# Optimization experiments

Measured on AMD Instinct MI355X. Metric: run time of the kernel, lower is better.

Reference implementation:

```python
import jax, jax.numpy as jnp
import numpy as np

D_MODEL = 2048
NUM_HEADS = 16
HEAD_DIM = D_MODEL // NUM_HEADS
SEQ = 2048
BATCH = 2
ROPE_BASE = 10000.0
EPS = 1e-5


def _rope_cache(seq_len, head_dim, base):
    inv_freq = 1.0 / (base ** (jnp.arange(0, head_dim, 2, dtype=jnp.float32) / head_dim))
    t = jnp.arange(seq_len, dtype=jnp.float32)
    freqs = jnp.outer(t, inv_freq)                      # [S, hd/2]
    emb = jnp.concatenate([freqs, freqs], axis=-1)      # [S, hd]
    return jnp.cos(emb), jnp.sin(emb)


def _rotate_half(x):
    x1, x2 = jnp.split(x, 2, axis=-1)
    return jnp.concatenate([-x2, x1], axis=-1)


def setup_inputs() -> dict:
    key = jax.random.key(0)
    ks = jax.random.split(key, 8)
    s = 1.0 / np.sqrt(D_MODEL)
    inp = {
        "x": jax.random.normal(ks[0], (SEQ, BATCH, D_MODEL), dtype=jnp.float32),
        "causal_mask": jnp.triu(jnp.ones((SEQ, SEQ), dtype=jnp.bool_), k=1),
        "key_padding_mask": jnp.zeros((BATCH, SEQ), dtype=jnp.bool_),
        "norm_w": jnp.ones((D_MODEL,), dtype=jnp.float32),
        "q_w": jax.random.normal(ks[1], (D_MODEL, D_MODEL), dtype=jnp.float32) * s,
        "q_b": jnp.zeros((D_MODEL,), dtype=jnp.float32),
        "k_w": jax.random.normal(ks[2], (D_MODEL, D_MODEL), dtype=jnp.float32) * s,
        "k_b": jnp.zeros((D_MODEL,), dtype=jnp.float32),
        "v_w": jax.random.normal(ks[3], (D_MODEL, D_MODEL), dtype=jnp.float32) * s,
        "v_b": jnp.zeros((D_MODEL,), dtype=jnp.float32),
        "o_w": jax.random.normal(ks[4], (D_MODEL, D_MODEL), dtype=jnp.float32) * s,
        "o_b": jnp.zeros((D_MODEL,), dtype=jnp.float32),
    }
    return inp


def reference(x, causal_mask, key_padding_mask, norm_w, q_w, q_b, k_w, k_b, v_w, v_b, o_w, o_b):
    seq_len, batch, _ = x.shape
    # RMSNorm variant: x / (||x||_2 + eps) * w  (note: L2 norm, not RMS)
    nrm = jnp.linalg.norm(x, axis=-1, keepdims=True)
    xn = x / (nrm + EPS) * norm_w

    q = (xn @ q_w.T + q_b).reshape(seq_len, batch, NUM_HEADS, HEAD_DIM)
    k = (xn @ k_w.T + k_b).reshape(seq_len, batch, NUM_HEADS, HEAD_DIM)
    v = (xn @ v_w.T + v_b).reshape(seq_len, batch, NUM_HEADS, HEAD_DIM)

    cos, sin = _rope_cache(seq_len, HEAD_DIM, ROPE_BASE)
    cos = cos[:, None, None, :]
    sin = sin[:, None, None, :]
    q = q * cos + _rotate_half(q) * sin
    k = k * cos + _rotate_half(k) * sin

    # [S,B,H,D] -> [B,H,S,D]
    q = q.transpose(1, 2, 0, 3)
    k = k.transpose(1, 2, 0, 3)
    v = v.transpose(1, 2, 0, 3)

    scores = jnp.einsum('bhqd,bhkd->bhqk', q, k) / jnp.sqrt(jnp.float32(HEAD_DIM))
    neg_inf = jnp.float32(-jnp.inf)
    scores = jnp.where(causal_mask[None, None, :, :], neg_inf, scores)
    scores = jnp.where(key_padding_mask[:, None, None, :], neg_inf, scores)

    attn = jax.nn.softmax(scores, axis=-1)
    out = jnp.einsum('bhqk,bhkd->bhqd', attn, v)
    out = out.transpose(2, 0, 1, 3).reshape(seq_len, batch, D_MODEL)  # [S,B,D]
    return out @ o_w.T + o_b
```

## Files before the change

### kernel.cpp

```cpp
#include <hip/hip_runtime.h>
#include <hip/hip_bf16.h>
#include <cstdint>

typedef __attribute__((ext_vector_type(8))) short short8_t;
typedef __attribute__((ext_vector_type(4))) short s16x4;
typedef __attribute__((ext_vector_type(4))) float f32x4;

#define SEQ 2048
#define BATCH 2
#define DM 2048
#define NH 16
#define HD 128
#define SCALE 0.08838834764831845f

__device__ __forceinline__ short f2bf(float f) {
    union { __hip_bfloat16 h; short s; } u; u.h = __float2bfloat16(f); return u.s;
}
__device__ __forceinline__ float bf2f(short s) {
    union { short s; __hip_bfloat16 h; } u; u.s = s; return __bfloat162float(u.h);
}

__global__ void rope_table_kernel(float* __restrict__ cosT, float* __restrict__ sinT) {
    int t = blockIdx.x;
    int i = threadIdx.x;
    float inv = exp2f(-(2.0f * (float)i / 128.0f) * log2f(10000.0f));
    float a = (float)t * inv;
    cosT[t * 64 + i] = cosf(a);
    sinT[t * 64 + i] = sinf(a);
}

__global__ void cast4_kernel(const float* __restrict__ qw, const float* __restrict__ kw,
                             const float* __restrict__ vw, const float* __restrict__ ow,
                             short* __restrict__ out) {
    const int per = DM * DM / 4;
    int i = blockIdx.x * blockDim.x + threadIdx.x;
    int stride = gridDim.x * blockDim.x;
    for (; i < 4 * per; i += stride) {
        int region = i / per;
        int off = i - region * per;
        const float* src = region == 0 ? qw : (region == 1 ? kw : (region == 2 ? vw : ow));
        float4 v = ((const float4*)src)[off];
        s16x4 o;
        o[0] = f2bf(v.x); o[1] = f2bf(v.y); o[2] = f2bf(v.z); o[3] = f2bf(v.w);
        ((s16x4*)(out + (size_t)region * DM * DM))[off] = o;
    }
}

__global__ void __launch_bounds__(256) norm_cast_kernel(const float* __restrict__ x,
                                                        const float* __restrict__ w,
                                                        short* __restrict__ xn) {
    __shared__ float red[4];
    int row = blockIdx.x;
    const float* xr = x + (size_t)row * DM;
    short* outr = xn + (size_t)row * DM;
    int t = threadIdx.x;
    float vals[8];
    float ss = 0.f;
#pragma unroll
    for (int i = 0; i < 8; ++i) { float v = xr[t + 256 * i]; vals[i] = v; ss += v * v; }
#pragma unroll
    for (int off = 1; off < 64; off <<= 1) ss += __shfl_xor(ss, off);
    int lane = t & 63, wv = t >> 6;
    if (lane == 0) red[wv] = ss;
    __syncthreads();
    float tot = red[0] + red[1] + red[2] + red[3];
    float inv = 1.f / (sqrtf(tot) + 1e-5f);
#pragma unroll
    for (int i = 0; i < 8; ++i)
        outr[t + 256 * i] = f2bf(vals[i] * inv * w[t + 256 * i]);
}


__device__ __forceinline__ void stage64(const short* __restrict__ G, int gRow0, int K, int kb,
                                        short* dstLds, int w, int lane) {
#pragma unroll
    for (int p = 0; p < 4; ++p) {
        int c = p * 256 + w * 64 + lane;
        int row = c >> 3;
        int slot = (c & 7) ^ (row & 7);
        const short* g = G + (size_t)(gRow0 + row) * K + kb + slot * 8;
        __builtin_amdgcn_global_load_lds((const __attribute__((address_space(1))) void*)g,
                                         (__attribute__((address_space(3))) void*)(dstLds + (p * 256 + w * 64) * 8),
                                         16, 0, 0);
    }
}

template <int MODE>
__global__ void __launch_bounds__(256) gemm_bt2(const short* __restrict__ A,
                                                const short* __restrict__ B,
                                                int N, int K,
                                                short* __restrict__ oq, short* __restrict__ ok,
                                                short* __restrict__ ov,
                                                const float* __restrict__ bq,
                                                const float* __restrict__ bk,
                                                const float* __restrict__ bv,
                                                float* __restrict__ outF,
                                                const float* __restrict__ bias) {
    __shared__ short As[128 * 64];
    __shared__ short Bs[128 * 64];
    const int tid = threadIdx.x;
    const int lane = tid & 63;
    const int w = tid >> 6;
    const int wr = w >> 1, wc = w & 1;
    const int brow = blockIdx.y * 128;
    const int bcol = blockIdx.x * 128;

    f32x4 acc[4][4];
#pragma unroll
    for (int i = 0; i < 4; ++i)
#pragma unroll
        for (int j = 0; j < 4; ++j) acc[i][j] = (f32x4){0.f, 0.f, 0.f, 0.f};

    const int fr = lane & 15;
    const int fs = lane >> 4;

    for (int kb = 0; kb < K; kb += 64) {
        stage64(A, brow, K, kb, As, w, lane);
        stage64(B, bcol, K, kb, Bs, w, lane);
        __syncthreads();

        short8_t af[4][2], bfv[4][2];
#pragma unroll
        for (int i = 0; i < 4; ++i) {
            int ar = wr * 64 + i * 16 + fr;
#pragma unroll
            for (int ks = 0; ks < 2; ++ks)
                af[i][ks] = *(const short8_t*)&As[ar * 64 + ((ks * 4 + fs) ^ (fr & 7)) * 8];
        }
#pragma unroll
        for (int j = 0; j < 4; ++j) {
            int br = wc * 64 + j * 16 + fr;
#pragma unroll
            for (int ks = 0; ks < 2; ++ks)
                bfv[j][ks] = *(const short8_t*)&Bs[br * 64 + ((ks * 4 + fs) ^ (fr & 7)) * 8];
        }
#pragma unroll
        for (int ks = 0; ks < 2; ++ks)
#pragma unroll
            for (int i = 0; i < 4; ++i)
#pragma unroll
                for (int j = 0; j < 4; ++j)
                    acc[i][j] = __builtin_amdgcn_mfma_f32_16x16x32_bf16(af[i][ks], bfv[j][ks], acc[i][j], 0, 0, 0);
        __syncthreads();
    }

    const int fq = (lane >> 4) * 4;
#pragma unroll
    for (int i = 0; i < 4; ++i) {
        int mrow = brow + wr * 64 + i * 16 + fq;
#pragma unroll
        for (int j = 0; j < 4; ++j) {
            int ncol = bcol + wc * 64 + j * 16 + fr;
            if (MODE == 0) {
                int which = ncol >> 11;
                int hl = ncol & 2047;
                int h = hl >> 7, d = hl & 127;
                const float* bp = which == 0 ? bq : (which == 1 ? bk : bv);
                short* dst = which == 0 ? oq : (which == 1 ? ok : ov);
                float bval = bp[hl];
#pragma unroll
                for (int jj = 0; jj < 4; ++jj) {
                    int m = mrow + jj;
                    int s = m >> 1, b = m & 1;
                    float v = acc[i][j][jj] + bval;
                    size_t idx;
                    if (which == 2)
                        idx = (((size_t)(b * NH + h)) * HD + d) * SEQ + s;
                    else
                        idx = (((size_t)(b * NH + h)) * SEQ + s) * HD + d;
                    dst[idx] = f2bf(v);
                }
            } else {
                float bval = bias[ncol];
#pragma unroll
                for (int jj = 0; jj < 4; ++jj) {
                    int m = mrow + jj;
                    outF[(size_t)m * N + ncol] = acc[i][j][jj] + bval;
                }
            }
        }
    }
}

__global__ void __launch_bounds__(256) rope_kernel(short* __restrict__ q, short* __restrict__ k,
                                                   const float* __restrict__ cosT,
                                                   const float* __restrict__ sinT) {
    int w = threadIdx.x >> 6, lane = threadIdx.x & 63;
    int idx = blockIdx.x * 4 + w;
    int s = idx & (SEQ - 1);
    size_t base = (size_t)idx * HD;
    float c = cosT[s * 64 + lane], sn = sinT[s * 64 + lane];
    float q1 = bf2f(q[base + lane]), q2 = bf2f(q[base + lane + 64]);
    q[base + lane] = f2bf(q1 * c - q2 * sn);
    q[base + lane + 64] = f2bf(q2 * c + q1 * sn);
    float k1 = bf2f(k[base + lane]), k2 = bf2f(k[base + lane + 64]);
    k[base + lane] = f2bf(k1 * c - k2 * sn);
    k[base + lane + 64] = f2bf(k2 * c + k1 * sn);
}

__global__ void __launch_bounds__(512) attn_kernel(const short* __restrict__ Q,
                                                   const short* __restrict__ K,
                                                   const short* __restrict__ V,
                                                   short* __restrict__ AO) {
    __shared__ short Kl[64 * 136];
    __shared__ short Vt[128 * 88];
    __shared__ short Pl[8][16 * 88];

    const int bh = blockIdx.x;
    const int qt = blockIdx.y;
    const int b = bh >> 4;
    const int h = bh & 15;
    const size_t base = (size_t)bh * (SEQ * HD);
    const int tid = threadIdx.x;
    const int lane = tid & 63;
    const int w = tid >> 6;
    const int fr = lane & 15;
    const int fk = (lane >> 4) * 8;
    const int fq = (lane >> 4) * 4;
    const int qbase = qt * 128 + w * 16;
    const int qg = qbase + fr;

    short8_t qf[4];
#pragma unroll
    for (int kc = 0; kc < 4; ++kc)
        qf[kc] = *(const short8_t*)&Q[base + (size_t)(qbase + fr) * HD + kc * 32 + fk];

    f32x4 acc[8];
#pragma unroll
    for (int dt = 0; dt < 8; ++dt) acc[dt] = (f32x4){0.f, 0.f, 0.f, 0.f};
    float m_r = -1e30f, l_r = 0.f;

    const int ktmax = qt * 2 + 1;
    for (int kt = 0; kt <= ktmax; ++kt) {
#pragma unroll
        for (int p = 0; p < 2; ++p) {
            int idx = p * 512 + tid;
            int r = idx >> 4;
            int c8 = (idx & 15) * 8;
            *(short8_t*)&Kl[r * 136 + c8] =
                *(const short8_t*)&K[base + (size_t)(kt * 64 + r) * HD + c8];
        }
#pragma unroll
        for (int p = 0; p < 2; ++p) {
            int idx = p * 512 + tid;
            int d = idx >> 3;
            int c8 = (idx & 7) * 8;
            *(short8_t*)&Vt[d * 88 + c8] =
                *(const short8_t*)&V[base + (size_t)d * SEQ + kt * 64 + c8];
        }
        __syncthreads();

        if (kt * 64 <= qbase + 15) {
            f32x4 st[4];
#pragma unroll
            for (int nt = 0; nt < 4; ++nt) {
                f32x4 a = (f32x4){0.f, 0.f, 0.f, 0.f};
#pragma unroll
                for (int kc = 0; kc < 4; ++kc) {
                    short8_t kf = *(const short8_t*)&Kl[(nt * 16 + fr) * 136 + kc * 32 + fk];
                    a = __builtin_amdgcn_mfma_f32_16x16x32_bf16(kf, qf[kc], a, 0, 0, 0);
                }
                st[nt] = a;
            }

            float rmax = -1e30f;
#pragma unroll
            for (int nt = 0; nt < 4; ++nt) {
#pragma unroll
                for (int jj = 0; jj < 4; ++jj) {
                    int kg = kt * 64 + nt * 16 + fq + jj;
                    float sv = st[nt][jj];
                    sv = (kg > qg) ? -1e30f : sv;
                    st[nt][jj] = sv;
                    rmax = fmaxf(rmax, sv);
                }
            }
            rmax = fmaxf(rmax, __shfl_xor(rmax, 16));
            rmax = fmaxf(rmax, __shfl_xor(rmax, 32));
            float m_new = fmaxf(m_r, rmax);
            float corr = __expf((m_r - m_new) * SCALE);
            float rsum = 0.f;
#pragma unroll
            for (int nt = 0; nt < 4; ++nt) {
                s16x4 pk;
#pragma unroll
                for (int jj = 0; jj < 4; ++jj) {
                    float p = __expf((st[nt][jj] - m_new) * SCALE);
                    rsum += p;
                    pk[jj] = f2bf(p);
                }
                *(s16x4*)&Pl[w][fr * 88 + nt * 16 + fq] = pk;
            }
            rsum += __shfl_xor(rsum, 16);
            rsum += __shfl_xor(rsum, 32);
            l_r = l_r * corr + rsum;
            m_r = m_new;

            float c4[4];
#pragma unroll
            for (int jj = 0; jj < 4; ++jj) c4[jj] = __shfl(corr, fq + jj);
#pragma unroll
            for (int dt = 0; dt < 8; ++dt) {
#pragma unroll
                for (int jj = 0; jj < 4; ++jj) acc[dt][jj] *= c4[jj];
            }

#pragma unroll
            for (int kc = 0; kc < 2; ++kc) {
                short8_t pf = *(const short8_t*)&Pl[w][fr * 88 + kc * 32 + fk];
#pragma unroll
                for (int dt = 0; dt < 8; ++dt) {
                    short8_t vf = *(const short8_t*)&Vt[(dt * 16 + fr) * 88 + kc * 32 + fk];
                    acc[dt] = __builtin_amdgcn_mfma_f32_16x16x32_bf16(pf, vf, acc[dt], 0, 0, 0);
                }
            }
        }
        __syncthreads();
    }

    float linv[4];
#pragma unroll
    for (int jj = 0; jj < 4; ++jj) linv[jj] = 1.f / __shfl(l_r, fq + jj);
#pragma unroll
    for (int dt = 0; dt < 8; ++dt) {
#pragma unroll
        for (int jj = 0; jj < 4; ++jj) {
            int qrow = qbase + fq + jj;
            int d = dt * 16 + fr;
            AO[((size_t)(qrow * BATCH + b)) * DM + h * HD + d] = f2bf(acc[dt][jj] * linv[jj]);
        }
    }
}

extern "C" void kernel_launch(void* const* d_in, const int* in_sizes, int n_in,
                              void* d_out, int out_size, void* d_ws, size_t ws_size,
                              hipStream_t stream) {
    (void)in_sizes; (void)n_in; (void)out_size; (void)ws_size;
    const float* x  = (const float*)d_in[0];
    const float* nw = (const float*)d_in[3];
    const float* qw = (const float*)d_in[4];
    const float* qbias = (const float*)d_in[5];
    const float* kw = (const float*)d_in[6];
    const float* kbias = (const float*)d_in[7];
    const float* vw = (const float*)d_in[8];
    const float* vbias = (const float*)d_in[9];
    const float* ow = (const float*)d_in[10];
    const float* obias = (const float*)d_in[11];
    float* out = (float*)d_out;

    char* ws = (char*)d_ws;
    size_t off = 0;
    float* cosT = (float*)(ws + off); off += (size_t)SEQ * 64 * 4;
    float* sinT = (float*)(ws + off); off += (size_t)SEQ * 64 * 4;
    short* wqkv = (short*)(ws + off); off += (size_t)3 * DM * DM * 2;
    short* wo   = (short*)(ws + off); off += (size_t)DM * DM * 2;
    short* xn   = (short*)(ws + off); off += (size_t)SEQ * BATCH * DM * 2;
    short* qd   = (short*)(ws + off); off += (size_t)SEQ * BATCH * DM * 2;
    short* kd   = (short*)(ws + off); off += (size_t)SEQ * BATCH * DM * 2;
    short* vd   = (short*)(ws + off); off += (size_t)SEQ * BATCH * DM * 2;
    short* ao   = xn;

    rope_table_kernel<<<SEQ, 64, 0, stream>>>(cosT, sinT);
    cast4_kernel<<<2048, 256, 0, stream>>>(qw, kw, vw, ow, wqkv);
    norm_cast_kernel<<<SEQ * BATCH, 256, 0, stream>>>(x, nw, xn);
    gemm_bt2<0><<<dim3(3 * DM / 128, SEQ * BATCH / 128), 256, 0, stream>>>(
        xn, wqkv, 3 * DM, DM, qd, kd, vd, qbias, kbias, vbias, nullptr, nullptr);
    rope_kernel<<<BATCH * NH * SEQ / 4, 256, 0, stream>>>(qd, kd, cosT, sinT);
    attn_kernel<<<dim3(BATCH * NH, SEQ / 128), 512, 0, stream>>>(qd, kd, vd, ao);
    gemm_bt2<1><<<dim3(DM / 128, SEQ * BATCH / 128), 256, 0, stream>>>(
        ao, wo, DM, DM, nullptr, nullptr, nullptr, nullptr, nullptr, nullptr, out, obias);
}
```

Baseline: 300.2 us.

## Fuse prep kernels, prefetch K/V tiles, fold softmax scale, skip masks and rescales

Merges the rope-table, weight-cast and norm-cast kernels into one launch. In attention it prefetches the next K/V tile into registers while the current tile computes, raises wave priority around the MFMA blocks, and folds the softmax scale into Q during RoPE. It applies the causal mask only on diagonal tiles and skips the accumulator rescale when the running max grows by at most a threshold. These target launch overhead, exposed global-load latency and softmax ALU work, at the cost of more registers and a lazy-rescale bound that could reduce exp range safety.

Measured after the change: 280.5 us. 1.07x faster.

```diff
diff --git a/kernel.cpp b/kernel.cpp
--- a/kernel.cpp
+++ b/kernel.cpp
@@ -20,56 +20,59 @@
     union { short s; __hip_bfloat16 h; } u; u.s = s; return __bfloat162float(u.h);
 }
 
-__global__ void rope_table_kernel(float* __restrict__ cosT, float* __restrict__ sinT) {
-    int t = blockIdx.x;
-    int i = threadIdx.x;
-    float inv = exp2f(-(2.0f * (float)i / 128.0f) * log2f(10000.0f));
-    float a = (float)t * inv;
-    cosT[t * 64 + i] = cosf(a);
-    sinT[t * 64 + i] = sinf(a);
-}
-
-__global__ void cast4_kernel(const float* __restrict__ qw, const float* __restrict__ kw,
-                             const float* __restrict__ vw, const float* __restrict__ ow,
-                             short* __restrict__ out) {
-    const int per = DM * DM / 4;
-    int i = blockIdx.x * blockDim.x + threadIdx.x;
-    int stride = gridDim.x * blockDim.x;
-    for (; i < 4 * per; i += stride) {
-        int region = i / per;
-        int off = i - region * per;
-        const float* src = region == 0 ? qw : (region == 1 ? kw : (region == 2 ? vw : ow));
-        float4 v = ((const float4*)src)[off];
-        s16x4 o;
-        o[0] = f2bf(v.x); o[1] = f2bf(v.y); o[2] = f2bf(v.z); o[3] = f2bf(v.w);
-        ((s16x4*)(out + (size_t)region * DM * DM))[off] = o;
-    }
-}
-
-__global__ void __launch_bounds__(256) norm_cast_kernel(const float* __restrict__ x,
-                                                        const float* __restrict__ w,
-                                                        short* __restrict__ xn) {
-    __shared__ float red[4];
-    int row = blockIdx.x;
-    const float* xr = x + (size_t)row * DM;
-    short* outr = xn + (size_t)row * DM;
-    int t = threadIdx.x;
-    float vals[8];
-    float ss = 0.f;
-#pragma unroll
-    for (int i = 0; i < 8; ++i) { float v = xr[t + 256 * i]; vals[i] = v; ss += v * v; }
-#pragma unroll
-    for (int off = 1; off < 64; off <<= 1) ss += __shfl_xor(ss, off);
-    int lane = t & 63, wv = t >> 6;
-    if (lane == 0) red[wv] = ss;
-    __syncthreads();
-    float tot = red[0] + red[1] + red[2] + red[3];
-    float inv = 1.f / (sqrtf(tot) + 1e-5f);
-#pragma unroll
-    for (int i = 0; i < 8; ++i)
-        outr[t + 256 * i] = f2bf(vals[i] * inv * w[t + 256 * i]);
-}
-
+__global__ void __launch_bounds__(256) prep_kernel(const float* __restrict__ qw,
+                                                   const float* __restrict__ kw,
+                                                   const float* __restrict__ vw,
+                                                   const float* __restrict__ ow,
+                                                   short* __restrict__ wqkv,
+                                                   const float* __restrict__ x,
+                                                   const float* __restrict__ nw,
+                                                   short* __restrict__ xn,
+                                                   float* __restrict__ cosT,
+                                                   float* __restrict__ sinT) {
+    const int bid = blockIdx.x;
+    const int t = threadIdx.x;
+    if (bid < 2048) {
+        const int per = DM * DM / 4;
+        int i = bid * 256 + t;
+        const int stride = 2048 * 256;
+        for (; i < 4 * per; i += stride) {
+            int region = i / per;
+            int off = i - region * per;
+            const float* src = region == 0 ? qw : (region == 1 ? kw : (region == 2 ? vw : ow));
+            float4 v = ((const float4*)src)[off];
+            s16x4 o;
+            o[0] = f2bf(v.x); o[1] = f2bf(v.y); o[2] = f2bf(v.z); o[3] = f2bf(v.w);
+            ((s16x4*)(wqkv + (size_t)region * DM * DM))[off] = o;
+        }
+    } else if (bid < 2560) {
+        int j = (bid - 2048) * 256 + t;
+        int tpos = j >> 6, i = j & 63;
+        float inv = exp2f(-(2.0f * (float)i / 128.0f) * log2f(10000.0f));
+        float a = (float)tpos * inv;
+        cosT[tpos * 64 + i] = cosf(a);
+        sinT[tpos * 64 + i] = sinf(a);
+    } else {
+        __shared__ float red[4];
+        int row = bid - 2560;
+        const float* xr = x + (size_t)row * DM;
+        short* outr = xn + (size_t)row * DM;
+        float vals[8];
+        float ss = 0.f;
+#pragma unroll
+        for (int i = 0; i < 8; ++i) { float v = xr[t + 256 * i]; vals[i] = v; ss += v * v; }
+#pragma unroll
+        for (int off = 1; off < 64; off <<= 1) ss += __shfl_xor(ss, off);
+        int lane = t & 63, wv = t >> 6;
+        if (lane == 0) red[wv] = ss;
+        __syncthreads();
+        float tot = red[0] + red[1] + red[2] + red[3];
+        float inv = 1.f / (sqrtf(tot) + 1e-5f);
+#pragma unroll
+        for (int i = 0; i < 8; ++i)
+            outr[t + 256 * i] = f2bf(vals[i] * inv * nw[t + 256 * i]);
+    }
+}
 
 __device__ __forceinline__ void stage64(const short* __restrict__ G, int gRow0, int K, int kb,
                                         short* dstLds, int w, int lane) {
@@ -191,8 +194,8 @@
     size_t base = (size_t)idx * HD;
     float c = cosT[s * 64 + lane], sn = sinT[s * 64 + lane];
     float q1 = bf2f(q[base + lane]), q2 = bf2f(q[base + lane + 64]);
-    q[base + lane] = f2bf(q1 * c - q2 * sn);
-    q[base + lane + 64] = f2bf(q2 * c + q1 * sn);
+    q[base + lane] = f2bf((q1 * c - q2 * sn) * SCALE);
+    q[base + lane + 64] = f2bf((q2 * c + q1 * sn) * SCALE);
     float k1 = bf2f(k[base + lane]), k2 = bf2f(k[base + lane + 64]);
     k[base + lane] = f2bf(k1 * c - k2 * sn);
     k[base + lane + 64] = f2bf(k2 * c + k1 * sn);
@@ -220,6 +223,11 @@
     const int qbase = qt * 128 + w * 16;
     const int qg = qbase + fr;
 
+    const int kr = tid >> 4;
+    const int kc8 = (tid & 15) * 8;
+    const int vd = tid >> 3;
+    const int vc8 = (tid & 7) * 8;
+
     short8_t qf[4];
 #pragma unroll
     for (int kc = 0; kc < 4; ++kc)
@@ -231,27 +239,25 @@
     float m_r = -1e30f, l_r = 0.f;
 
     const int ktmax = qt * 2 + 1;
+
+    short8_t kreg[2], vreg[2];
+#pragma unroll
+    for (int p = 0; p < 2; ++p) {
+        kreg[p] = *(const short8_t*)&K[base + (size_t)(p * 32 + kr) * HD + kc8];
+        vreg[p] = *(const short8_t*)&V[base + (size_t)(p * 64 + vd) * SEQ + vc8];
+    }
+#pragma unroll
+    for (int p = 0; p < 2; ++p) {
+        *(short8_t*)&Kl[(p * 32 + kr) * 136 + kc8] = kreg[p];
+        *(short8_t*)&Vt[(p * 64 + vd) * 88 + vc8] = vreg[p];
+    }
+    __syncthreads();
+
     for (int kt = 0; kt <= ktmax; ++kt) {
-#pragma unroll
-        for (int p = 0; p < 2; ++p) {
-            int idx = p * 512 + tid;
-            int r = idx >> 4;
-            int c8 = (idx & 15) * 8;
-            *(short8_t*)&Kl[r * 136 + c8] =
-                *(const short8_t*)&K[base + (size_t)(kt * 64 + r) * HD + c8];
-        }
-#pragma unroll
-        for (int p = 0; p < 2; ++p) {
-            int idx = p * 512 + tid;
-            int d = idx >> 3;
-            int c8 = (idx & 7) * 8;
-            *(short8_t*)&Vt[d * 88 + c8] =
-                *(const short8_t*)&V[base + (size_t)d * SEQ + kt * 64 + c8];
-        }
-        __syncthreads();
-
-        if (kt * 64 <= qbase + 15) {
-            f32x4 st[4];
+        const bool active = (kt * 64 <= qbase + 15);
+        f32x4 st[4];
+        if (active) {
+            __builtin_amdgcn_s_setprio(1);
 #pragma unroll
             for (int nt = 0; nt < 4; ++nt) {
                 f32x4 a = (f32x4){0.f, 0.f, 0.f, 0.f};
@@ -262,30 +268,51 @@
                 }
                 st[nt] = a;
             }
-
+            __builtin_amdgcn_s_setprio(0);
+        }
+
+        if (kt < ktmax) {
+            const size_t kb2 = base + (size_t)((kt + 1) * 64) * HD;
+            const size_t vb2 = base + (size_t)(kt + 1) * 64;
+#pragma unroll
+            for (int p = 0; p < 2; ++p) {
+                kreg[p] = *(const short8_t*)&K[kb2 + (size_t)(p * 32 + kr) * HD + kc8];
+                vreg[p] = *(const short8_t*)&V[vb2 + (size_t)(p * 64 + vd) * SEQ + vc8];
+            }
+        }
+
+        if (active) {
+            const bool needMask = (kt * 64 + 63 > qbase);
             float rmax = -1e30f;
-#pragma unroll
-            for (int nt = 0; nt < 4; ++nt) {
-#pragma unroll
-                for (int jj = 0; jj < 4; ++jj) {
-                    int kg = kt * 64 + nt * 16 + fq + jj;
-                    float sv = st[nt][jj];
-                    sv = (kg > qg) ? -1e30f : sv;
-                    st[nt][jj] = sv;
-                    rmax = fmaxf(rmax, sv);
-                }
+            if (needMask) {
+#pragma unroll
+                for (int nt = 0; nt < 4; ++nt)
+#pragma unroll
+                    for (int jj = 0; jj < 4; ++jj) {
+                        int kg = kt * 64 + nt * 16 + fq + jj;
+                        float sv = st[nt][jj];
+                        sv = (kg > qg) ? -1e30f : sv;
+                        st[nt][jj] = sv;
+                        rmax = fmaxf(rmax, sv);
+                    }
+            } else {
+#pragma unroll
+                for (int nt = 0; nt < 4; ++nt)
+#pragma unroll
+                    for (int jj = 0; jj < 4; ++jj) rmax = fmaxf(rmax, st[nt][jj]);
             }
             rmax = fmaxf(rmax, __shfl_xor(rmax, 16));
             rmax = fmaxf(rmax, __shfl_xor(rmax, 32));
-            float m_new = fmaxf(m_r, rmax);
-            float corr = __expf((m_r - m_new) * SCALE);
+
+            const bool doRescale = !(m_r > -1e29f && __all(rmax - m_r <= 8.0f));
+            float m_new = doRescale ? fmaxf(m_r, rmax) : m_r;
             float rsum = 0.f;
 #pragma unroll
             for (int nt = 0; nt < 4; ++nt) {
                 s16x4 pk;
 #pragma unroll
                 for (int jj = 0; jj < 4; ++jj) {
-                    float p = __expf((st[nt][jj] - m_new) * SCALE);
+                    float p = __expf(st[nt][jj] - m_new);
                     rsum += p;
                     pk[jj] = f2bf(p);
                 }
@@ -293,18 +320,22 @@
             }
             rsum += __shfl_xor(rsum, 16);
             rsum += __shfl_xor(rsum, 32);
-            l_r = l_r * corr + rsum;
-            m_r = m_new;
-
-            float c4[4];
-#pragma unroll
-            for (int jj = 0; jj < 4; ++jj) c4[jj] = __shfl(corr, fq + jj);
-#pragma unroll
-            for (int dt = 0; dt < 8; ++dt) {
-#pragma unroll
-                for (int jj = 0; jj < 4; ++jj) acc[dt][jj] *= c4[jj];
-            }
-
+            if (doRescale) {
+                float corr = __expf(m_r - m_new);
+                l_r = l_r * corr + rsum;
+                m_r = m_new;
+                float c4[4];
+#pragma unroll
+                for (int jj = 0; jj < 4; ++jj) c4[jj] = __shfl(corr, fq + jj);
+#pragma unroll
+                for (int dt = 0; dt < 8; ++dt)
+#pragma unroll
+                    for (int jj = 0; jj < 4; ++jj) acc[dt][jj] *= c4[jj];
+            } else {
+                l_r += rsum;
+            }
+
+            __builtin_amdgcn_s_setprio(1);
 #pragma unroll
             for (int kc = 0; kc < 2; ++kc) {
                 short8_t pf = *(const short8_t*)&Pl[w][fr * 88 + kc * 32 + fk];
@@ -314,8 +345,18 @@
                     acc[dt] = __builtin_amdgcn_mfma_f32_16x16x32_bf16(pf, vf, acc[dt], 0, 0, 0);
                 }
             }
-        }
+            __builtin_amdgcn_s_setprio(0);
+        }
+
         __syncthreads();
+        if (kt < ktmax) {
+#pragma unroll
+            for (int p = 0; p < 2; ++p) {
+                *(short8_t*)&Kl[(p * 32 + kr) * 136 + kc8] = kreg[p];
+                *(short8_t*)&Vt[(p * 64 + vd) * 88 + vc8] = vreg[p];
+            }
+            __syncthreads();
+        }
     }
 
     float linv[4];
@@ -360,9 +401,7 @@
     short* vd   = (short*)(ws + off); off += (size_t)SEQ * BATCH * DM * 2;
     short* ao   = xn;
 
-    rope_table_kernel<<<SEQ, 64, 0, stream>>>(cosT, sinT);
-    cast4_kernel<<<2048, 256, 0, stream>>>(qw, kw, vw, ow, wqkv);
-    norm_cast_kernel<<<SEQ * BATCH, 256, 0, stream>>>(x, nw, xn);
+    prep_kernel<<<2560 + SEQ * BATCH, 256, 0, stream>>>(qw, kw, vw, ow, wqkv, x, nw, xn, cosT, sinT);
     gemm_bt2<0><<<dim3(3 * DM / 128, SEQ * BATCH / 128), 256, 0, stream>>>(
         xn, wqkv, 3 * DM, DM, qd, kd, vd, qbias, kbias, vbias, nullptr, nullptr);
     rope_kernel<<<BATCH * NH * SEQ / 4, 256, 0, stream>>>(qd, kd, cosT, sinT);
```
